# Performance work log

Measured on AMD Instinct MI355X. Metric: run time of the kernel, lower is better.

## Reference

```python
import jax, jax.numpy as jnp
import numpy as np

BS, L, DIM, H, POS = 2, 2048, 1024, 16, 16
DH = DIM // H
SCALE = float(np.round(np.sqrt(DH), 2))  # torch code: np.round(np.sqrt(d_head), 2)


def setup_inputs() -> dict:
    key = jax.random.key(0)
    ks = jax.random.split(key, 12)
    init = lambda k, shape: (jax.random.normal(k, shape, dtype=jnp.float32) * 0.02)
    inp = {
        "q": jax.random.normal(ks[0], (BS, L, DIM + POS), dtype=jnp.float32),
        "k": jax.random.normal(ks[1], (BS, L, DIM + POS), dtype=jnp.float32),
        "v": jax.random.normal(ks[2], (BS, L, DIM + POS), dtype=jnp.float32),
        "Wq": init(ks[3], (DIM, DIM)), "bq": jnp.zeros((DIM,), jnp.float32),
        "Wk": init(ks[4], (DIM, DIM)), "bk": jnp.zeros((DIM,), jnp.float32),
        "Wv": init(ks[5], (DIM, DIM)), "bv": jnp.zeros((DIM,), jnp.float32),
        "Wo": init(ks[6], (DIM, DIM)), "bo": jnp.zeros((DIM,), jnp.float32),
        # causal mask: positions with mask==1 are filled with -1e9 (strict upper triangle)
        "attn_mask": jnp.triu(jnp.ones((L, L), jnp.int32), k=1),
        "pos_token_dim": POS,
    }
    return inp


def reference(q, k, v, Wq, bq, Wk, bk, Wv, bv, Wo, bo, attn_mask, pos_token_dim):
    # pos-token suffix: stripped from q/k/v; encoding taken from k's suffix
    encoding = k[..., -pos_token_dim:]                      # [bs, L, pos]
    q = q[..., :-pos_token_dim]
    k = k[..., :-pos_token_dim]
    v = v[..., :-pos_token_dim]
    bs, Ln, dim = q.shape
    h, dh = H, DH

    # QKV projections (torch Linear: x @ W.T + b), split into heads -> [bs, h, L, dh]
    queries = (q @ Wq.T + bq).reshape(bs, Ln, h, dh).transpose(0, 2, 1, 3)
    keys    = (k @ Wk.T + bk).reshape(bs, Ln, h, dh).transpose(0, 2, 1, 3)
    values  = (v @ Wv.T + bv).reshape(bs, Ln, h, dh).transpose(0, 2, 1, 3)

    # full L x L score matrix (faithful to original naive attention)
    scores = jnp.einsum("bhld,bhmd->bhlm", queries, keys) / SCALE
    scores = jnp.where(attn_mask[None, None, :, :] == 1, jnp.float32(-1e9), scores)
    factors = jax.nn.softmax(scores, axis=-1)               # [bs, h, L, L]

    context = jnp.einsum("bhlm,bhmd->bhld", factors, values)
    context = context.transpose(0, 2, 1, 3).reshape(bs, Ln, dim)
    context = context @ Wo.T + bo                           # [bs, L, dim]

    # pos-token passthrough: attend encoding with same factors, mean over heads
    context_encoding = jnp.einsum("bhlm,bmp->bhlp", factors, encoding).mean(axis=1)
    return jnp.concatenate([context, context_encoding], axis=-1)  # [bs, L, dim+pos]
```

## Files before the change

### kernel.cpp

```cpp
#include <hip/hip_runtime.h>
#include <hip/hip_bf16.h>

#define BS   2
#define LEN  2048
#define DIM  1024
#define NH   16
#define DHD  64
#define POSD 16
#define DHE  80
#define NTOK 4096
#define INW  1040

typedef __attribute__((ext_vector_type(8))) short bf16x8;
typedef __attribute__((ext_vector_type(4))) float f32x4;

__device__ __forceinline__ short f2bf(float f) {
    union { float f; unsigned u; } v; v.f = f;
    unsigned r = v.u + 0x7fffu + ((v.u >> 16) & 1u);
    return (short)(r >> 16);
}
__device__ __forceinline__ float bf2f(short s) {
    union { unsigned u; float f; } v; v.u = ((unsigned)(unsigned short)s) << 16;
    return v.f;
}
__device__ __forceinline__ unsigned packbf(float a, float b) {
    union { float f; unsigned u; } x, y; x.f = a; y.f = b;
    return ((x.u + 0x8000u) >> 16) | ((y.u + 0x8000u) & 0xFFFF0000u);
}
__device__ __forceinline__ f32x4 mfma16(bf16x8 a, bf16x8 b, f32x4 c) {
    return __builtin_amdgcn_mfma_f32_16x16x32_bf16(a, b, c, 0, 0, 0);
}
__device__ __forceinline__ void gld16(const short* g, short* l) {
    __builtin_amdgcn_global_load_lds(
        (const __attribute__((address_space(1))) unsigned int*)g,
        (__attribute__((address_space(3))) unsigned int*)l,
        16, 0, 0);
}

__global__ __launch_bounds__(256) void prep_kernel(
    const float* __restrict__ qin, const float* __restrict__ kin, const float* __restrict__ vin,
    const float* __restrict__ Wq, const float* __restrict__ Wk,
    const float* __restrict__ Wv, const float* __restrict__ Wo,
    short* __restrict__ X16, short* __restrict__ W16, short* __restrict__ Vt)
{
    const int NA = 3 * NTOK * DIM / 4;
    const int NW = 4 * DIM * DIM / 4;
    int idx = blockIdx.x * 256 + threadIdx.x;
    if (idx < NA) {
        int per = NTOK * DIM / 4;
        int mi = idx / per, r = idx % per;
        int tok = r >> 8, c4 = r & 255;
        const float* src = (mi == 0 ? qin : (mi == 1 ? kin : vin));
        float4 v = *(const float4*)(src + (size_t)tok * INW + c4 * 4);
        short4 o;
        o.x = f2bf(v.x); o.y = f2bf(v.y); o.z = f2bf(v.z); o.w = f2bf(v.w);
        *(short4*)(X16 + (size_t)mi * NTOK * DIM + (size_t)tok * DIM + c4 * 4) = o;
        return;
    }
    idx -= NA;
    if (idx < NW) {
        int wi = idx >> 18, r = idx & 262143;
        const float* w = (wi == 0 ? Wq : (wi == 1 ? Wk : (wi == 2 ? Wv : Wo)));
        float4 v = *(const float4*)(w + (size_t)r * 4);
        short4 o;
        o.x = f2bf(v.x); o.y = f2bf(v.y); o.z = f2bf(v.z); o.w = f2bf(v.w);
        *(short4*)(W16 + (size_t)wi * DIM * DIM + (size_t)r * 4) = o;
        return;
    }
    idx -= NW;
    if (idx < BS * NH * POSD * (LEN / 8)) {
        int l8 = idx & 255;
        int p  = (idx >> 8) & 15;
        int h  = (idx >> 12) & 15;
        int b  = (idx >> 16);
        int l0 = l8 * 8;
        bf16x8 o;
        for (int i = 0; i < 8; i++)
            o[i] = f2bf(kin[(size_t)(b * LEN + l0 + i) * INW + DIM + p]);
        *(bf16x8*)(Vt + ((size_t)(b * NH + h) * DHE + DHD + p) * LEN + l0) = o;
    }
}

__global__ __launch_bounds__(256) void qkv_gemm(
    const short* __restrict__ X16, const short* __restrict__ W16,
    const float* __restrict__ bq, const float* __restrict__ bk, const float* __restrict__ bv,
    short* __restrict__ Qb, short* __restrict__ Kb, short* __restrict__ Vt)
{
    __shared__ __align__(16) short smem[24576];

    int sw = (blockIdx.x & 7) * 96 + (blockIdx.x >> 3);
    int nt = sw % 24, mt = sw / 24;
    int mat = nt >> 3, ntl = nt & 7;
    const short* A = X16 + (size_t)mat * NTOK * DIM;
    const short* W = W16 + (size_t)mat * DIM * DIM;

    int t = threadIdx.x;
    int w = t >> 6, lane = t & 63, g = lane >> 4, c = lane & 15;
    int wr = w >> 1, wc = w & 1;

    f32x4 acc[4][4];
    #pragma unroll
    for (int i = 0; i < 4; i++)
        #pragma unroll
        for (int j = 0; j < 4; j++)
            acc[i][j] = (f32x4){0.f, 0.f, 0.f, 0.f};

    int row0 = t >> 2, blk0 = t & 3;
    const short* aSrc0 = A + (size_t)(mt * 128 + row0) * DIM + blk0 * 8;
    const short* aSrc1 = aSrc0 + (size_t)64 * DIM;
    const short* bSrc0 = W + (size_t)(ntl * 128 + row0) * DIM + blk0 * 8;
    const short* bSrc1 = bSrc0 + (size_t)64 * DIM;

    short* bufC  = smem;
    short* bufN  = smem + 8192;
    short* bufNN = smem + 16384;

    {
        short* ab = bufC + w * 512;
        gld16(aSrc0, ab);
        gld16(aSrc1, ab + 2048);
        gld16(bSrc0, ab + 4096);
        gld16(bSrc1, ab + 6144);
        ab = bufN + w * 512;
        gld16(aSrc0 + 32, ab);
        gld16(aSrc1 + 32, ab + 2048);
        gld16(bSrc0 + 32, ab + 4096);
        gld16(bSrc1 + 32, ab + 6144);
    }

    for (int k = 0; k < 32; k++) {
        if (k < 30) {
            int k0 = (k + 2) * 32;
            short* ab = bufNN + w * 512;
            gld16(aSrc0 + k0, ab);
            gld16(aSrc1 + k0, ab + 2048);
            gld16(bSrc0 + k0, ab + 4096);
            gld16(bSrc1 + k0, ab + 6144);
            asm volatile("s_waitcnt vmcnt(8)" ::: "memory");
        } else if (k == 30) {
            asm volatile("s_waitcnt vmcnt(4)" ::: "memory");
        } else {
            asm volatile("s_waitcnt vmcnt(0)" ::: "memory");
        }
        __builtin_amdgcn_s_barrier();
        asm volatile("" ::: "memory");

        const short* Asb = bufC;
        const short* Bsb = bufC + 4096;
        bf16x8 af[4], bfr[4];
        #pragma unroll
        for (int fm = 0; fm < 4; fm++)
            af[fm] = *(const bf16x8*)(Asb + (wr * 64 + fm * 16 + c) * 32 + g * 8);
        #pragma unroll
        for (int fn = 0; fn < 4; fn++)
            bfr[fn] = *(const bf16x8*)(Bsb + (wc * 64 + fn * 16 + c) * 32 + g * 8);
        __builtin_amdgcn_s_setprio(1);
        #pragma unroll
        for (int fm = 0; fm < 4; fm++)
            #pragma unroll
            for (int fn = 0; fn < 4; fn++)
                acc[fm][fn] = mfma16(af[fm], bfr[fn], acc[fm][fn]);
        __builtin_amdgcn_s_setprio(0);

        asm volatile("s_waitcnt lgkmcnt(0)" ::: "memory");
        __builtin_amdgcn_s_barrier();
        asm volatile("" ::: "memory");

        short* tmp = bufC; bufC = bufN; bufN = bufNN; bufNN = tmp;
    }

    const float* bias = (mat == 0 ? bq : (mat == 1 ? bk : bv));
    if (mat == 2) {
        __syncthreads();
        #pragma unroll
        for (int fn = 0; fn < 4; fn++) {
            int nl = wc * 64 + fn * 16 + c;
            float bval = bias[ntl * 128 + nl];
            #pragma unroll
            for (int fm = 0; fm < 4; fm++) {
                int m0 = wr * 64 + fm * 16 + g * 4;
                short4 pk;
                pk.x = f2bf(acc[fm][fn][0] + bval);
                pk.y = f2bf(acc[fm][fn][1] + bval);
                pk.z = f2bf(acc[fm][fn][2] + bval);
                pk.w = f2bf(acc[fm][fn][3] + bval);
                *(short4*)(smem + nl * 136 + m0) = pk;
            }
        }
        __syncthreads();
        int b_ = (mt * 128) >> 11;
        int l0 = (mt * 128) & 2047;
        #pragma unroll
        for (int rep = 0; rep < 8; rep++) {
            int idx = rep * 256 + t;
            int row = idx >> 4, ch = idx & 15;
            bf16x8 v = *(const bf16x8*)(smem + row * 136 + ch * 8);
            int ng = ntl * 128 + row, h = ng >> 6, dh = ng & 63;
            *(bf16x8*)(Vt + ((size_t)(b_ * NH + h) * DHE + dh) * LEN + l0 + ch * 8) = v;
        }
    } else {
        float qs = (mat == 0) ? 0.18033688011112042f : 1.0f;
        short* dst = (mat == 0) ? Qb : Kb;
        #pragma unroll
        for (int fn = 0; fn < 4; fn++) {
            int n = ntl * 128 + wc * 64 + fn * 16 + c;
            float bval = bias[n];
            int h = n >> 6, dh = n & 63;
            #pragma unroll
            for (int fm = 0; fm < 4; fm++) {
                int mbase = mt * 128 + wr * 64 + fm * 16 + g * 4;
                #pragma unroll
                for (int i = 0; i < 4; i++) {
                    int m = mbase + i;
                    int b_ = m >> 11, l = m & 2047;
                    dst[((size_t)(b_ * NH + h) * LEN + l) * DHD + dh] =
                        f2bf((acc[fm][fn][i] + bval) * qs);
                }
            }
        }
    }
}

__global__ __launch_bounds__(256) void attn_kernel(
    const short* __restrict__ Qb, const short* __restrict__ Kb,
    const short* __restrict__ Vt, short* __restrict__ Ctx)
{
    __shared__ __align__(16) short Ks[64 * 64];
    __shared__ __align__(16) short Vs[DHE * 64];
    __shared__ __align__(16) short Ps[4][16 * 64];

    int bid = blockIdx.x;
    int u = bid >> 5, bh = bid & 31;
    int qt = (u < 16) ? (2 * u) : (63 - 2 * u);
    int b = bh >> 4, h = bh & 15;
    int q0 = qt * 64;
    int t = threadIdx.x, w = t >> 6, lane = t & 63, g = lane >> 4, c = lane & 15;
    const size_t bhQ = (size_t)(b * NH + h) * LEN;
    const size_t bhV = (size_t)(b * NH + h) * DHE;

    bf16x8 qa0, qa1;
    {
        const short* qp = Qb + (bhQ + q0 + w * 16 + c) * DHD;
        qa0 = *(const bf16x8*)(qp + g * 8);
        qa1 = *(const bf16x8*)(qp + 32 + g * 8);
    }

    int rK = t >> 3, blkS = t & 7;
    int swzS = (blkS ^ (rK & 7)) * 8;
    short* kDst0 = Ks + rK * 64 + swzS;
    short* kDst1 = Ks + (rK + 32) * 64 + swzS;
    short* vDst0 = Vs + rK * 64 + swzS;
    short* vDst1 = Vs + (rK + 32) * 64 + swzS;
    short* vDst2 = Vs + (rK + 64) * 64 + swzS;
    const short* kS0 = Kb + (bhQ + rK) * DHD + blkS * 8;
    const short* kS1 = Kb + (bhQ + rK + 32) * DHD + blkS * 8;
    const short* vS0 = Vt + (bhV + rK) * LEN + blkS * 8;
    const short* vS1 = Vt + (bhV + rK + 32) * LEN + blkS * 8;
    const short* vS2 = Vt + (bhV + rK + 64) * LEN + blkS * 8;
    bool v2on = (t < 128);

    {
        bf16x8 a0 = *(const bf16x8*)kS0;
        bf16x8 a1 = *(const bf16x8*)kS1;
        bf16x8 x0 = *(const bf16x8*)vS0;
        bf16x8 x1 = *(const bf16x8*)vS1;
        bf16x8 x2;
        if (v2on) x2 = *(const bf16x8*)vS2;
        *(bf16x8*)kDst0 = a0;
        *(bf16x8*)kDst1 = a1;
        *(bf16x8*)vDst0 = x0;
        *(bf16x8*)vDst1 = x1;
        if (v2on) *(bf16x8*)vDst2 = x2;
    }
    __syncthreads();

    float mrun = -1e30f, lrun = 0.f;
    f32x4 o[5];
    #pragma unroll
    for (int i = 0; i < 5; i++) o[i] = (f32x4){0.f, 0.f, 0.f, 0.f};

    for (int tt = 0; tt <= qt; tt++) {
        bf16x8 kr0, kr1, vr0, vr1, vr2;
        bool pref = (tt < qt);
        if (pref) {
            int kvn = (tt + 1) * 64;
            kr0 = *(const bf16x8*)(kS0 + (size_t)kvn * DHD);
            kr1 = *(const bf16x8*)(kS1 + (size_t)kvn * DHD);
            vr0 = *(const bf16x8*)(vS0 + kvn);
            vr1 = *(const bf16x8*)(vS1 + kvn);
            if (v2on) vr2 = *(const bf16x8*)(vS2 + kvn);
        }

        f32x4 st[4];
        __builtin_amdgcn_s_setprio(1);
        #pragma unroll
        for (int fn = 0; fn < 4; fn++) {
            int row = fn * 16 + c, sw2 = row & 7;
            bf16x8 ka = *(const bf16x8*)(Ks + row * 64 + ((g ^ sw2) * 8));
            bf16x8 kb2 = *(const bf16x8*)(Ks + row * 64 + (((4 + g) ^ sw2) * 8));
            f32x4 z = (f32x4){0.f, 0.f, 0.f, 0.f};
            z = mfma16(ka, qa0, z);
            z = mfma16(kb2, qa1, z);
            st[fn] = z;
        }
        __builtin_amdgcn_s_setprio(0);

        if (tt == qt) {
            #pragma unroll
            for (int fn = 0; fn < 4; fn++)
                #pragma unroll
                for (int i = 0; i < 4; i++)
                    if (fn * 16 + g * 4 + i > w * 16 + c) st[fn][i] = -1e9f;
        }

        float mx = st[0][0];
        #pragma unroll
        for (int fn = 0; fn < 4; fn++)
            #pragma unroll
            for (int i = 0; i < 4; i++)
                mx = fmaxf(mx, st[fn][i]);
        mx = fmaxf(mx, __shfl_xor(mx, 16));
        mx = fmaxf(mx, __shfl_xor(mx, 32));
        float mnew = fmaxf(mrun, mx);
        float scl = __builtin_amdgcn_exp2f(mrun - mnew);
        mrun = mnew;
        float ps = 0.f;
        #pragma unroll
        for (int fn = 0; fn < 4; fn++)
            #pragma unroll
            for (int i = 0; i < 4; i++) {
                float p = __builtin_amdgcn_exp2f(st[fn][i] - mnew);
                st[fn][i] = p;
                ps += p;
            }
        ps += __shfl_xor(ps, 16);
        ps += __shfl_xor(ps, 32);
        lrun = lrun * scl + ps;

        short* pw = Ps[w];
        #pragma unroll
        for (int fn = 0; fn < 4; fn++) {
            uint2 pu;
            pu.x = packbf(st[fn][0], st[fn][1]);
            pu.y = packbf(st[fn][2], st[fn][3]);
            *(uint2*)(pw + c * 64 + ((((fn << 1) | (g >> 1)) ^ (c & 7)) << 3) + ((g & 1) << 2)) = pu;
        }
        bf16x8 pa0 = *(const bf16x8*)(pw + c * 64 + ((g ^ (c & 7)) * 8));
        bf16x8 pa1 = *(const bf16x8*)(pw + c * 64 + (((4 + g) ^ (c & 7)) * 8));

        float s0 = __shfl(scl, g * 4 + 0);
        float s1 = __shfl(scl, g * 4 + 1);
        float s2 = __shfl(scl, g * 4 + 2);
        float s3 = __shfl(scl, g * 4 + 3);
        #pragma unroll
        for (int fd = 0; fd < 5; fd++) {
            o[fd][0] *= s0; o[fd][1] *= s1; o[fd][2] *= s2; o[fd][3] *= s3;
        }

        __builtin_amdgcn_s_setprio(1);
        #pragma unroll
        for (int fd = 0; fd < 5; fd++) {
            int d = fd * 16 + c, sw2 = d & 7;
            bf16x8 vb0 = *(const bf16x8*)(Vs + d * 64 + ((g ^ sw2) * 8));
            bf16x8 vb1 = *(const bf16x8*)(Vs + d * 64 + (((4 + g) ^ sw2) * 8));
            o[fd] = mfma16(pa0, vb0, o[fd]);
            o[fd] = mfma16(pa1, vb1, o[fd]);
        }
        __builtin_amdgcn_s_setprio(0);

        __syncthreads();
        if (pref) {
            *(bf16x8*)kDst0 = kr0;
            *(bf16x8*)kDst1 = kr1;
            *(bf16x8*)vDst0 = vr0;
            *(bf16x8*)vDst1 = vr1;
            if (v2on) *(bf16x8*)vDst2 = vr2;
        }
        __syncthreads();
    }

    float l0 = __shfl(lrun, g * 4 + 0);
    float l1 = __shfl(lrun, g * 4 + 1);
    float l2 = __shfl(lrun, g * 4 + 2);
    float l3 = __shfl(lrun, g * 4 + 3);
    float inv[4] = {1.f / l0, 1.f / l1, 1.f / l2, 1.f / l3};
    #pragma unroll
    for (int i = 0; i < 4; i++) {
        int q = q0 + w * 16 + g * 4 + i;
        size_t base = (bhQ + q) * DHE;
        #pragma unroll
        for (int fd = 0; fd < 5; fd++)
            Ctx[base + fd * 16 + c] = f2bf(o[fd][i] * inv[i]);
    }
}

__global__ __launch_bounds__(256) void out_gemm(
    const short* __restrict__ Ctx, const short* __restrict__ Wo16,
    const float* __restrict__ bo, float* __restrict__ out)
{
    __shared__ __align__(16) short smem[24576];

    int sw = (blockIdx.x & 7) * 32 + (blockIdx.x >> 3);
    int nt = sw & 7, mt = sw >> 3;
    int t = threadIdx.x;
    int w = t >> 6, lane = t & 63, g = lane >> 4, c = lane & 15;
    int wr = w >> 1, wc = w & 1;

    f32x4 acc[4][4];
    #pragma unroll
    for (int i = 0; i < 4; i++)
        #pragma unroll
        for (int j = 0; j < 4; j++)
            acc[i][j] = (f32x4){0.f, 0.f, 0.f, 0.f};

    int row0 = t >> 2, blk0 = t & 3;
    int tokS = mt * 128 + row0;
    int bS = tokS >> 11, lS = tokS & 2047;
    const short* aBase = Ctx + ((size_t)(bS * NH) * LEN + lS) * DHE + blk0 * 8;
    const short* aBase1 = Ctx + ((size_t)(((tokS + 64) >> 11) * NH) * LEN + ((tokS + 64) & 2047)) * DHE + blk0 * 8;
    const short* bSrc0 = Wo16 + (size_t)(nt * 128 + row0) * DIM + blk0 * 8;
    const short* bSrc1 = bSrc0 + (size_t)64 * DIM;

    short* bufC  = smem;
    short* bufN  = smem + 8192;
    short* bufNN = smem + 16384;

    {
        short* ab = bufC + w * 512;
        gld16(aBase, ab);
        gld16(aBase1, ab + 2048);
        gld16(bSrc0, ab + 4096);
        gld16(bSrc1, ab + 6144);
        ab = bufN + w * 512;
        gld16(aBase + 32, ab);
        gld16(aBase1 + 32, ab + 2048);
        gld16(bSrc0 + 32, ab + 4096);
        gld16(bSrc1 + 32, ab + 6144);
    }

    for (int k = 0; k < 32; k++) {
        if (k < 30) {
            int k0 = (k + 2) * 32;
            size_t aoff = (size_t)(k0 >> 6) * LEN * DHE + (k0 & 63);
            short* ab = bufNN + w * 512;
            gld16(aBase + aoff, ab);
            gld16(aBase1 + aoff, ab + 2048);
            gld16(bSrc0 + k0, ab + 4096);
            gld16(bSrc1 + k0, ab + 6144);
            asm volatile("s_waitcnt vmcnt(8)" ::: "memory");
        } else if (k == 30) {
            asm volatile("s_waitcnt vmcnt(4)" ::: "memory");
        } else {
            asm volatile("s_waitcnt vmcnt(0)" ::: "memory");
        }
        __builtin_amdgcn_s_barrier();
        asm volatile("" ::: "memory");

        const short* Asb = bufC;
        const short* Bsb = bufC + 4096;
        bf16x8 af[4], bfr[4];
        #pragma unroll
        for (int fm = 0; fm < 4; fm++)
            af[fm] = *(const bf16x8*)(Asb + (wr * 64 + fm * 16 + c) * 32 + g * 8);
        #pragma unroll
        for (int fn = 0; fn < 4; fn++)
            bfr[fn] = *(const bf16x8*)(Bsb + (wc * 64 + fn * 16 + c) * 32 + g * 8);
        __builtin_amdgcn_s_setprio(1);
        #pragma unroll
        for (int fm = 0; fm < 4; fm++)
            #pragma unroll
            for (int fn = 0; fn < 4; fn++)
                acc[fm][fn] = mfma16(af[fm], bfr[fn], acc[fm][fn]);
        __builtin_amdgcn_s_setprio(0);

        asm volatile("s_waitcnt lgkmcnt(0)" ::: "memory");
        __builtin_amdgcn_s_barrier();
        asm volatile("" ::: "memory");

        short* tmp = bufC; bufC = bufN; bufN = bufNN; bufNN = tmp;
    }

    #pragma unroll
    for (int fn = 0; fn < 4; fn++) {
        int n = nt * 128 + wc * 64 + fn * 16 + c;
        float bval = bo[n];
        #pragma unroll
        for (int fm = 0; fm < 4; fm++) {
            int mbase = mt * 128 + wr * 64 + fm * 16 + g * 4;
            #pragma unroll
            for (int i = 0; i < 4; i++)
                out[(size_t)(mbase + i) * INW + n] = acc[fm][fn][i] + bval;
        }
    }
}

__global__ __launch_bounds__(256) void encmean_kernel(
    const short* __restrict__ Ctx, float* __restrict__ out)
{
    int idx = blockIdx.x * 256 + threadIdx.x;
    int tok = idx >> 4, p = idx & 15;
    int b = tok >> 11, l = tok & 2047;
    float s = 0.f;
    #pragma unroll
    for (int h = 0; h < NH; h++)
        s += bf2f(Ctx[((size_t)(b * NH + h) * LEN + l) * DHE + DHD + p]);
    out[(size_t)tok * INW + DIM + p] = s * (1.0f / NH);
}

extern "C" void kernel_launch(void* const* d_in, const int* in_sizes, int n_in,
                              void* d_out, int out_size, void* d_ws, size_t ws_size,
                              hipStream_t stream)
{
    const float* qin = (const float*)d_in[0];
    const float* kin = (const float*)d_in[1];
    const float* vin = (const float*)d_in[2];
    const float* Wq  = (const float*)d_in[3];
    const float* bq  = (const float*)d_in[4];
    const float* Wk  = (const float*)d_in[5];
    const float* bk  = (const float*)d_in[6];
    const float* Wv  = (const float*)d_in[7];
    const float* bv  = (const float*)d_in[8];
    const float* Wo  = (const float*)d_in[9];
    const float* bo  = (const float*)d_in[10];
    float* out = (float*)d_out;

    short* X16 = (short*)d_ws;
    short* W16 = X16 + (size_t)3 * NTOK * DIM;
    short* Qb  = W16 + (size_t)4 * DIM * DIM;
    short* Kb  = Qb  + (size_t)NTOK * DIM;
    short* Vt  = Kb  + (size_t)NTOK * DIM;
    short* Ctx = Vt  + (size_t)BS * NH * DHE * LEN;

    prep_kernel<<<16896, 256, 0, stream>>>(qin, kin, vin, Wq, Wk, Wv, Wo, X16, W16, Vt);
    qkv_gemm<<<768, 256, 0, stream>>>(X16, W16, bq, bk, bv, Qb, Kb, Vt);
    attn_kernel<<<1024, 256, 0, stream>>>(Qb, Kb, Vt, Ctx);
    out_gemm<<<256, 256, 0, stream>>>(Ctx, W16 + (size_t)3 * DIM * DIM, bo, out);
    encmean_kernel<<<256, 256, 0, stream>>>(Ctx, out);
}
```

Measured before the change: 132.6 us.

## Restructure attention so each wave owns 32 query rows and reads K/V from global

Attention is reorganised so each wave works independently on 32 query rows, two 16-row sub-tiles, of its own (batch, head). The wave loads K and V fragments straight from global memory into registers and prefetches the next tile itself, so the shared-memory K/V staging and both block-wide barriers per iteration are gone. The grid is halved and launch bounds now ask for two blocks per CU. Waves in a block now serve different heads and query tiles, so K/V data is no longer shared through LDS and global/L2 traffic per FLOP rises; register pressure also grows with the doubled accumulators and the register-held K/V.

Result: slower. 183.9 us (+38.7%).

```diff
diff --git a/kernel.cpp b/kernel.cpp
--- a/kernel.cpp
+++ b/kernel.cpp
@@ -221,176 +221,182 @@
     }
 }
 
-__global__ __launch_bounds__(256) void attn_kernel(
+__global__ __launch_bounds__(256, 2) void attn_kernel(
     const short* __restrict__ Qb, const short* __restrict__ Kb,
     const short* __restrict__ Vt, short* __restrict__ Ctx)
 {
-    __shared__ __align__(16) short Ks[64 * 64];
-    __shared__ __align__(16) short Vs[DHE * 64];
-    __shared__ __align__(16) short Ps[4][16 * 64];
+    __shared__ __align__(16) short Ps[4][2048];
 
     int bid = blockIdx.x;
-    int u = bid >> 5, bh = bid & 31;
-    int qt = (u < 16) ? (2 * u) : (63 - 2 * u);
+    int p = 31 - (bid >> 4);
+    int bhp = bid & 15;
+    int t = threadIdx.x, w = t >> 6, lane = t & 63, g = lane >> 4, c = lane & 15;
+    int bh = bhp + ((w & 1) << 4);
+    int W = 2 * p + (w >> 1);
     int b = bh >> 4, h = bh & 15;
-    int q0 = qt * 64;
-    int t = threadIdx.x, w = t >> 6, lane = t & 63, g = lane >> 4, c = lane & 15;
+    int wq0 = W * 32;
+    int T = p + 1;
     const size_t bhQ = (size_t)(b * NH + h) * LEN;
     const size_t bhV = (size_t)(b * NH + h) * DHE;
-
-    bf16x8 qa0, qa1;
-    {
-        const short* qp = Qb + (bhQ + q0 + w * 16 + c) * DHD;
-        qa0 = *(const bf16x8*)(qp + g * 8);
-        qa1 = *(const bf16x8*)(qp + 32 + g * 8);
-    }
-
-    int rK = t >> 3, blkS = t & 7;
-    int swzS = (blkS ^ (rK & 7)) * 8;
-    short* kDst0 = Ks + rK * 64 + swzS;
-    short* kDst1 = Ks + (rK + 32) * 64 + swzS;
-    short* vDst0 = Vs + rK * 64 + swzS;
-    short* vDst1 = Vs + (rK + 32) * 64 + swzS;
-    short* vDst2 = Vs + (rK + 64) * 64 + swzS;
-    const short* kS0 = Kb + (bhQ + rK) * DHD + blkS * 8;
-    const short* kS1 = Kb + (bhQ + rK + 32) * DHD + blkS * 8;
-    const short* vS0 = Vt + (bhV + rK) * LEN + blkS * 8;
-    const short* vS1 = Vt + (bhV + rK + 32) * LEN + blkS * 8;
-    const short* vS2 = Vt + (bhV + rK + 64) * LEN + blkS * 8;
-    bool v2on = (t < 128);
-
-    {
-        bf16x8 a0 = *(const bf16x8*)kS0;
-        bf16x8 a1 = *(const bf16x8*)kS1;
-        bf16x8 x0 = *(const bf16x8*)vS0;
-        bf16x8 x1 = *(const bf16x8*)vS1;
-        bf16x8 x2;
-        if (v2on) x2 = *(const bf16x8*)vS2;
-        *(bf16x8*)kDst0 = a0;
-        *(bf16x8*)kDst1 = a1;
-        *(bf16x8*)vDst0 = x0;
-        *(bf16x8*)vDst1 = x1;
-        if (v2on) *(bf16x8*)vDst2 = x2;
-    }
-    __syncthreads();
-
-    float mrun = -1e30f, lrun = 0.f;
-    f32x4 o[5];
-    #pragma unroll
-    for (int i = 0; i < 5; i++) o[i] = (f32x4){0.f, 0.f, 0.f, 0.f};
-
-    for (int tt = 0; tt <= qt; tt++) {
-        bf16x8 kr0, kr1, vr0, vr1, vr2;
-        bool pref = (tt < qt);
-        if (pref) {
+    short* pw = Ps[w];
+
+    bf16x8 qa[2][2];
+    #pragma unroll
+    for (int h2 = 0; h2 < 2; h2++)
+        #pragma unroll
+        for (int ks = 0; ks < 2; ks++)
+            qa[h2][ks] = *(const bf16x8*)(Qb + (bhQ + wq0 + h2 * 16 + c) * DHD + ks * 32 + g * 8);
+
+    const short* kB = Kb + (bhQ + c) * DHD + g * 8;
+    const short* vB = Vt + (bhV + c) * LEN + g * 8;
+
+    bf16x8 ka[4][2], vb[5][2];
+    #pragma unroll
+    for (int fn = 0; fn < 4; fn++)
+        #pragma unroll
+        for (int ks = 0; ks < 2; ks++)
+            ka[fn][ks] = *(const bf16x8*)(kB + (size_t)(fn * 16) * DHD + ks * 32);
+    #pragma unroll
+    for (int fd = 0; fd < 5; fd++)
+        #pragma unroll
+        for (int ks = 0; ks < 2; ks++)
+            vb[fd][ks] = *(const bf16x8*)(vB + (size_t)(fd * 16) * LEN + ks * 32);
+
+    float mrun[2] = {-1e30f, -1e30f}, lrun[2] = {0.f, 0.f};
+    f32x4 o[2][5];
+    #pragma unroll
+    for (int h2 = 0; h2 < 2; h2++)
+        #pragma unroll
+        for (int fd = 0; fd < 5; fd++)
+            o[h2][fd] = (f32x4){0.f, 0.f, 0.f, 0.f};
+
+    for (int tt = 0; tt < T; tt++) {
+        f32x4 st[2][4];
+        __builtin_amdgcn_s_setprio(1);
+        #pragma unroll
+        for (int h2 = 0; h2 < 2; h2++)
+            #pragma unroll
+            for (int fn = 0; fn < 4; fn++) {
+                f32x4 z = (f32x4){0.f, 0.f, 0.f, 0.f};
+                z = mfma16(ka[fn][0], qa[h2][0], z);
+                z = mfma16(ka[fn][1], qa[h2][1], z);
+                st[h2][fn] = z;
+            }
+        __builtin_amdgcn_s_setprio(0);
+
+        if (tt + 1 < T) {
             int kvn = (tt + 1) * 64;
-            kr0 = *(const bf16x8*)(kS0 + (size_t)kvn * DHD);
-            kr1 = *(const bf16x8*)(kS1 + (size_t)kvn * DHD);
-            vr0 = *(const bf16x8*)(vS0 + kvn);
-            vr1 = *(const bf16x8*)(vS1 + kvn);
-            if (v2on) vr2 = *(const bf16x8*)(vS2 + kvn);
-        }
-
-        f32x4 st[4];
-        __builtin_amdgcn_s_setprio(1);
-        #pragma unroll
-        for (int fn = 0; fn < 4; fn++) {
-            int row = fn * 16 + c, sw2 = row & 7;
-            bf16x8 ka = *(const bf16x8*)(Ks + row * 64 + ((g ^ sw2) * 8));
-            bf16x8 kb2 = *(const bf16x8*)(Ks + row * 64 + (((4 + g) ^ sw2) * 8));
-            f32x4 z = (f32x4){0.f, 0.f, 0.f, 0.f};
-            z = mfma16(ka, qa0, z);
-            z = mfma16(kb2, qa1, z);
-            st[fn] = z;
-        }
-        __builtin_amdgcn_s_setprio(0);
-
-        if (tt == qt) {
+            #pragma unroll
+            for (int fn = 0; fn < 4; fn++)
+                #pragma unroll
+                for (int ks = 0; ks < 2; ks++)
+                    ka[fn][ks] = *(const bf16x8*)(kB + (size_t)(kvn + fn * 16) * DHD + ks * 32);
+        }
+
+        if (tt == T - 1) {
+            #pragma unroll
+            for (int h2 = 0; h2 < 2; h2++)
+                #pragma unroll
+                for (int fn = 0; fn < 4; fn++)
+                    #pragma unroll
+                    for (int i = 0; i < 4; i++)
+                        if (tt * 64 + fn * 16 + g * 4 + i > wq0 + h2 * 16 + c)
+                            st[h2][fn][i] = -1e30f;
+        }
+
+        float scl[2];
+        #pragma unroll
+        for (int h2 = 0; h2 < 2; h2++) {
+            float mx = st[h2][0][0];
             #pragma unroll
             for (int fn = 0; fn < 4; fn++)
                 #pragma unroll
                 for (int i = 0; i < 4; i++)
-                    if (fn * 16 + g * 4 + i > w * 16 + c) st[fn][i] = -1e9f;
-        }
-
-        float mx = st[0][0];
-        #pragma unroll
-        for (int fn = 0; fn < 4; fn++)
-            #pragma unroll
-            for (int i = 0; i < 4; i++)
-                mx = fmaxf(mx, st[fn][i]);
-        mx = fmaxf(mx, __shfl_xor(mx, 16));
-        mx = fmaxf(mx, __shfl_xor(mx, 32));
-        float mnew = fmaxf(mrun, mx);
-        float scl = __builtin_amdgcn_exp2f(mrun - mnew);
-        mrun = mnew;
-        float ps = 0.f;
-        #pragma unroll
-        for (int fn = 0; fn < 4; fn++)
-            #pragma unroll
-            for (int i = 0; i < 4; i++) {
-                float p = __builtin_amdgcn_exp2f(st[fn][i] - mnew);
-                st[fn][i] = p;
-                ps += p;
+                    mx = fmaxf(mx, st[h2][fn][i]);
+            mx = fmaxf(mx, __shfl_xor(mx, 16));
+            mx = fmaxf(mx, __shfl_xor(mx, 32));
+            float mnew = fmaxf(mrun[h2], mx);
+            scl[h2] = __builtin_amdgcn_exp2f(mrun[h2] - mnew);
+            mrun[h2] = mnew;
+            float ps = 0.f;
+            #pragma unroll
+            for (int fn = 0; fn < 4; fn++)
+                #pragma unroll
+                for (int i = 0; i < 4; i++) {
+                    float pe = __builtin_amdgcn_exp2f(st[h2][fn][i] - mnew);
+                    st[h2][fn][i] = pe;
+                    ps += pe;
+                }
+            ps += __shfl_xor(ps, 16);
+            ps += __shfl_xor(ps, 32);
+            lrun[h2] = lrun[h2] * scl[h2] + ps;
+        }
+
+        #pragma unroll
+        for (int h2 = 0; h2 < 2; h2++)
+            #pragma unroll
+            for (int fn = 0; fn < 4; fn++) {
+                uint2 pu;
+                pu.x = packbf(st[h2][fn][0], st[h2][fn][1]);
+                pu.y = packbf(st[h2][fn][2], st[h2][fn][3]);
+                *(uint2*)(pw + (h2 * 16 + c) * 64 +
+                          ((((fn << 1) | (g >> 1)) ^ (c & 7)) << 3) + ((g & 1) << 2)) = pu;
             }
-        ps += __shfl_xor(ps, 16);
-        ps += __shfl_xor(ps, 32);
-        lrun = lrun * scl + ps;
-
-        short* pw = Ps[w];
-        #pragma unroll
-        for (int fn = 0; fn < 4; fn++) {
-            uint2 pu;
-            pu.x = packbf(st[fn][0], st[fn][1]);
-            pu.y = packbf(st[fn][2], st[fn][3]);
-            *(uint2*)(pw + c * 64 + ((((fn << 1) | (g >> 1)) ^ (c & 7)) << 3) + ((g & 1) << 2)) = pu;
-        }
-        bf16x8 pa0 = *(const bf16x8*)(pw + c * 64 + ((g ^ (c & 7)) * 8));
-        bf16x8 pa1 = *(const bf16x8*)(pw + c * 64 + (((4 + g) ^ (c & 7)) * 8));
-
-        float s0 = __shfl(scl, g * 4 + 0);
-        float s1 = __shfl(scl, g * 4 + 1);
-        float s2 = __shfl(scl, g * 4 + 2);
-        float s3 = __shfl(scl, g * 4 + 3);
-        #pragma unroll
-        for (int fd = 0; fd < 5; fd++) {
-            o[fd][0] *= s0; o[fd][1] *= s1; o[fd][2] *= s2; o[fd][3] *= s3;
+        bf16x8 pa[2][2];
+        #pragma unroll
+        for (int h2 = 0; h2 < 2; h2++) {
+            pa[h2][0] = *(const bf16x8*)(pw + (h2 * 16 + c) * 64 + ((g ^ (c & 7)) * 8));
+            pa[h2][1] = *(const bf16x8*)(pw + (h2 * 16 + c) * 64 + (((4 + g) ^ (c & 7)) * 8));
+        }
+
+        #pragma unroll
+        for (int h2 = 0; h2 < 2; h2++) {
+            float s0 = __shfl(scl[h2], g * 4 + 0);
+            float s1 = __shfl(scl[h2], g * 4 + 1);
+            float s2 = __shfl(scl[h2], g * 4 + 2);
+            float s3 = __shfl(scl[h2], g * 4 + 3);
+            #pragma unroll
+            for (int fd = 0; fd < 5; fd++) {
+                o[h2][fd][0] *= s0; o[h2][fd][1] *= s1;
+                o[h2][fd][2] *= s2; o[h2][fd][3] *= s3;
+            }
         }
 
         __builtin_amdgcn_s_setprio(1);
         #pragma unroll
-        for (int fd = 0; fd < 5; fd++) {
-            int d = fd * 16 + c, sw2 = d & 7;
-            bf16x8 vb0 = *(const bf16x8*)(Vs + d * 64 + ((g ^ sw2) * 8));
-            bf16x8 vb1 = *(const bf16x8*)(Vs + d * 64 + (((4 + g) ^ sw2) * 8));
-            o[fd] = mfma16(pa0, vb0, o[fd]);
-            o[fd] = mfma16(pa1, vb1, o[fd]);
-        }
+        for (int h2 = 0; h2 < 2; h2++)
+            #pragma unroll
+            for (int fd = 0; fd < 5; fd++) {
+                o[h2][fd] = mfma16(pa[h2][0], vb[fd][0], o[h2][fd]);
+                o[h2][fd] = mfma16(pa[h2][1], vb[fd][1], o[h2][fd]);
+            }
         __builtin_amdgcn_s_setprio(0);
 
-        __syncthreads();
-        if (pref) {
-            *(bf16x8*)kDst0 = kr0;
-            *(bf16x8*)kDst1 = kr1;
-            *(bf16x8*)vDst0 = vr0;
-            *(bf16x8*)vDst1 = vr1;
-            if (v2on) *(bf16x8*)vDst2 = vr2;
-        }
-        __syncthreads();
-    }
-
-    float l0 = __shfl(lrun, g * 4 + 0);
-    float l1 = __shfl(lrun, g * 4 + 1);
-    float l2 = __shfl(lrun, g * 4 + 2);
-    float l3 = __shfl(lrun, g * 4 + 3);
-    float inv[4] = {1.f / l0, 1.f / l1, 1.f / l2, 1.f / l3};
-    #pragma unroll
-    for (int i = 0; i < 4; i++) {
-        int q = q0 + w * 16 + g * 4 + i;
-        size_t base = (bhQ + q) * DHE;
-        #pragma unroll
-        for (int fd = 0; fd < 5; fd++)
-            Ctx[base + fd * 16 + c] = f2bf(o[fd][i] * inv[i]);
+        if (tt + 1 < T) {
+            int kvn = (tt + 1) * 64;
+            #pragma unroll
+            for (int fd = 0; fd < 5; fd++)
+                #pragma unroll
+                for (int ks = 0; ks < 2; ks++)
+                    vb[fd][ks] = *(const bf16x8*)(vB + (size_t)(fd * 16) * LEN + kvn + ks * 32);
+        }
+    }
+
+    #pragma unroll
+    for (int h2 = 0; h2 < 2; h2++) {
+        float l0 = __shfl(lrun[h2], g * 4 + 0);
+        float l1 = __shfl(lrun[h2], g * 4 + 1);
+        float l2 = __shfl(lrun[h2], g * 4 + 2);
+        float l3 = __shfl(lrun[h2], g * 4 + 3);
+        float inv[4] = {1.f / l0, 1.f / l1, 1.f / l2, 1.f / l3};
+        #pragma unroll
+        for (int i = 0; i < 4; i++) {
+            int q = wq0 + h2 * 16 + g * 4 + i;
+            size_t base = (bhQ + q) * DHE;
+            #pragma unroll
+            for (int fd = 0; fd < 5; fd++)
+                Ctx[base + fd * 16 + c] = f2bf(o[h2][fd][i] * inv[i]);
+        }
     }
 }
 
@@ -533,7 +539,7 @@
 
     prep_kernel<<<16896, 256, 0, stream>>>(qin, kin, vin, Wq, Wk, Wv, Wo, X16, W16, Vt);
     qkv_gemm<<<768, 256, 0, stream>>>(X16, W16, bq, bk, bv, Qb, Kb, Vt);
-    attn_kernel<<<1024, 256, 0, stream>>>(Qb, Kb, Vt, Ctx);
+    attn_kernel<<<512, 256, 0, stream>>>(Qb, Kb, Vt, Ctx);
     out_gemm<<<256, 256, 0, stream>>>(Ctx, W16 + (size_t)3 * DIM * DIM, bo, out);
     encmean_kernel<<<256, 256, 0, stream>>>(Ctx, out);
 }
```

## Rework attention onto 32x32 MFMA with register-resident P and lazy rescaling

Applied to the files above, without the earlier changes.

The attention kernel moves from 16x16x32 to 32x32x16 bf16 MFMA. Each block now has two waves, and each wave owns 32 query rows. The probability tile is repacked across lanes with cross-half shuffles instead of a round trip through LDS, and the online-softmax rescale of the accumulators is skipped unless the running max grows by more than 8. Query tiles are scheduled longest-first to shrink the tail, which in exchange brings fewer threads per block, higher register pressure and wasted MFMA work on padded V rows.

Result: slower. 182.1 us (+37.4%).

```diff
diff --git a/kernel.cpp b/kernel.cpp
--- a/kernel.cpp
+++ b/kernel.cpp
@@ -13,6 +13,8 @@
 
 typedef __attribute__((ext_vector_type(8))) short bf16x8;
 typedef __attribute__((ext_vector_type(4))) float f32x4;
+typedef __attribute__((ext_vector_type(16))) float f32x16;
+typedef __attribute__((ext_vector_type(4))) unsigned uint32x4;
 
 __device__ __forceinline__ short f2bf(float f) {
     union { float f; unsigned u; } v; v.f = f;
@@ -29,6 +31,9 @@
 }
 __device__ __forceinline__ f32x4 mfma16(bf16x8 a, bf16x8 b, f32x4 c) {
     return __builtin_amdgcn_mfma_f32_16x16x32_bf16(a, b, c, 0, 0, 0);
+}
+__device__ __forceinline__ f32x16 mfma32(bf16x8 a, bf16x8 b, f32x16 c) {
+    return __builtin_amdgcn_mfma_f32_32x32x16_bf16(a, b, c, 0, 0, 0);
 }
 __device__ __forceinline__ void gld16(const short* g, short* l) {
     __builtin_amdgcn_global_load_lds(
@@ -221,176 +226,211 @@
     }
 }
 
-__global__ __launch_bounds__(256) void attn_kernel(
+__global__ __launch_bounds__(128) void attn_kernel(
     const short* __restrict__ Qb, const short* __restrict__ Kb,
     const short* __restrict__ Vt, short* __restrict__ Ctx)
 {
     __shared__ __align__(16) short Ks[64 * 64];
-    __shared__ __align__(16) short Vs[DHE * 64];
-    __shared__ __align__(16) short Ps[4][16 * 64];
+    __shared__ __align__(16) short Vs[96 * 64];
 
     int bid = blockIdx.x;
     int u = bid >> 5, bh = bid & 31;
-    int qt = (u < 16) ? (2 * u) : (63 - 2 * u);
+    int qt = (u < 16) ? (31 - 2 * u) : (2 * u - 32);
     int b = bh >> 4, h = bh & 15;
     int q0 = qt * 64;
-    int t = threadIdx.x, w = t >> 6, lane = t & 63, g = lane >> 4, c = lane & 15;
+    int t = threadIdx.x, w = t >> 6, l = t & 63;
+    int q32 = l & 31, half = l >> 5;
+    int wq0 = q0 + w * 32;
+    int T = qt + 1;
     const size_t bhQ = (size_t)(b * NH + h) * LEN;
     const size_t bhV = (size_t)(b * NH + h) * DHE;
 
-    bf16x8 qa0, qa1;
+    bf16x8 qf[4];
+    #pragma unroll
+    for (int dks = 0; dks < 4; dks++)
+        qf[dks] = *(const bf16x8*)(Qb + (bhQ + wq0 + q32) * DHD + dks * 16 + half * 8);
+
+    int sr = t >> 3, sb = t & 7;
+    int ssw = (sb ^ (sr & 7)) * 8;
+    const short* kS0 = Kb + (bhQ + sr) * DHD + sb * 8;
+    const short* kS1 = kS0 + (size_t)16 * DHD;
+    const short* kS2 = kS0 + (size_t)32 * DHD;
+    const short* kS3 = kS0 + (size_t)48 * DHD;
+    short* kD0 = Ks + sr * 64 + ssw;
+    short* kD1 = kD0 + 16 * 64;
+    short* kD2 = kD0 + 32 * 64;
+    short* kD3 = kD0 + 48 * 64;
+    const short* vS0 = Vt + (bhV + sr) * LEN + sb * 8;
+    const short* vS1 = vS0 + (size_t)16 * LEN;
+    const short* vS2 = vS0 + (size_t)32 * LEN;
+    const short* vS3 = vS0 + (size_t)48 * LEN;
+    const short* vS4 = vS0 + (size_t)64 * LEN;
+    short* vD0 = Vs + sr * 64 + ssw;
+    short* vD1 = vD0 + 16 * 64;
+    short* vD2 = vD0 + 32 * 64;
+    short* vD3 = vD0 + 48 * 64;
+    short* vD4 = vD0 + 64 * 64;
+
     {
-        const short* qp = Qb + (bhQ + q0 + w * 16 + c) * DHD;
-        qa0 = *(const bf16x8*)(qp + g * 8);
-        qa1 = *(const bf16x8*)(qp + 32 + g * 8);
-    }
-
-    int rK = t >> 3, blkS = t & 7;
-    int swzS = (blkS ^ (rK & 7)) * 8;
-    short* kDst0 = Ks + rK * 64 + swzS;
-    short* kDst1 = Ks + (rK + 32) * 64 + swzS;
-    short* vDst0 = Vs + rK * 64 + swzS;
-    short* vDst1 = Vs + (rK + 32) * 64 + swzS;
-    short* vDst2 = Vs + (rK + 64) * 64 + swzS;
-    const short* kS0 = Kb + (bhQ + rK) * DHD + blkS * 8;
-    const short* kS1 = Kb + (bhQ + rK + 32) * DHD + blkS * 8;
-    const short* vS0 = Vt + (bhV + rK) * LEN + blkS * 8;
-    const short* vS1 = Vt + (bhV + rK + 32) * LEN + blkS * 8;
-    const short* vS2 = Vt + (bhV + rK + 64) * LEN + blkS * 8;
-    bool v2on = (t < 128);
-
-    {
-        bf16x8 a0 = *(const bf16x8*)kS0;
-        bf16x8 a1 = *(const bf16x8*)kS1;
-        bf16x8 x0 = *(const bf16x8*)vS0;
-        bf16x8 x1 = *(const bf16x8*)vS1;
-        bf16x8 x2;
-        if (v2on) x2 = *(const bf16x8*)vS2;
-        *(bf16x8*)kDst0 = a0;
-        *(bf16x8*)kDst1 = a1;
-        *(bf16x8*)vDst0 = x0;
-        *(bf16x8*)vDst1 = x1;
-        if (v2on) *(bf16x8*)vDst2 = x2;
+        bf16x8 a0 = *(const bf16x8*)kS0, a1 = *(const bf16x8*)kS1;
+        bf16x8 a2 = *(const bf16x8*)kS2, a3 = *(const bf16x8*)kS3;
+        bf16x8 x0 = *(const bf16x8*)vS0, x1 = *(const bf16x8*)vS1;
+        bf16x8 x2 = *(const bf16x8*)vS2, x3 = *(const bf16x8*)vS3;
+        bf16x8 x4 = *(const bf16x8*)vS4;
+        *(bf16x8*)kD0 = a0; *(bf16x8*)kD1 = a1;
+        *(bf16x8*)kD2 = a2; *(bf16x8*)kD3 = a3;
+        *(bf16x8*)vD0 = x0; *(bf16x8*)vD1 = x1;
+        *(bf16x8*)vD2 = x2; *(bf16x8*)vD3 = x3;
+        *(bf16x8*)vD4 = x4;
     }
     __syncthreads();
 
     float mrun = -1e30f, lrun = 0.f;
-    f32x4 o[5];
-    #pragma unroll
-    for (int i = 0; i < 5; i++) o[i] = (f32x4){0.f, 0.f, 0.f, 0.f};
-
-    for (int tt = 0; tt <= qt; tt++) {
-        bf16x8 kr0, kr1, vr0, vr1, vr2;
-        bool pref = (tt < qt);
+    f32x16 o0, o1, o2;
+    #pragma unroll
+    for (int r = 0; r < 16; r++) { o0[r] = 0.f; o1[r] = 0.f; o2[r] = 0.f; }
+
+    int swq = (q32 & 7);
+
+    for (int tt = 0; tt < T; tt++) {
+        int kv0 = tt * 64;
+        bf16x8 kr0, kr1, kr2, kr3, vr0, vr1, vr2, vr3, vr4;
+        bool pref = (tt + 1 < T);
         if (pref) {
-            int kvn = (tt + 1) * 64;
-            kr0 = *(const bf16x8*)(kS0 + (size_t)kvn * DHD);
-            kr1 = *(const bf16x8*)(kS1 + (size_t)kvn * DHD);
-            vr0 = *(const bf16x8*)(vS0 + kvn);
-            vr1 = *(const bf16x8*)(vS1 + kvn);
-            if (v2on) vr2 = *(const bf16x8*)(vS2 + kvn);
-        }
-
-        f32x4 st[4];
+            size_t ko = (size_t)(kv0 + 64) * DHD;
+            int vo = kv0 + 64;
+            kr0 = *(const bf16x8*)(kS0 + ko); kr1 = *(const bf16x8*)(kS1 + ko);
+            kr2 = *(const bf16x8*)(kS2 + ko); kr3 = *(const bf16x8*)(kS3 + ko);
+            vr0 = *(const bf16x8*)(vS0 + vo); vr1 = *(const bf16x8*)(vS1 + vo);
+            vr2 = *(const bf16x8*)(vS2 + vo); vr3 = *(const bf16x8*)(vS3 + vo);
+            vr4 = *(const bf16x8*)(vS4 + vo);
+        }
+
+        f32x16 s0, s1;
+        #pragma unroll
+        for (int r = 0; r < 16; r++) { s0[r] = 0.f; s1[r] = 0.f; }
         __builtin_amdgcn_s_setprio(1);
         #pragma unroll
-        for (int fn = 0; fn < 4; fn++) {
-            int row = fn * 16 + c, sw2 = row & 7;
-            bf16x8 ka = *(const bf16x8*)(Ks + row * 64 + ((g ^ sw2) * 8));
-            bf16x8 kb2 = *(const bf16x8*)(Ks + row * 64 + (((4 + g) ^ sw2) * 8));
-            f32x4 z = (f32x4){0.f, 0.f, 0.f, 0.f};
-            z = mfma16(ka, qa0, z);
-            z = mfma16(kb2, qa1, z);
-            st[fn] = z;
+        for (int dks = 0; dks < 4; dks++) {
+            int ch = dks * 2 + half;
+            bf16x8 ka0 = *(const bf16x8*)(Ks + q32 * 64 + ((ch ^ swq) * 8));
+            bf16x8 ka1 = *(const bf16x8*)(Ks + (32 + q32) * 64 + ((ch ^ swq) * 8));
+            s0 = mfma32(ka0, qf[dks], s0);
+            s1 = mfma32(ka1, qf[dks], s1);
         }
         __builtin_amdgcn_s_setprio(0);
 
-        if (tt == qt) {
-            #pragma unroll
-            for (int fn = 0; fn < 4; fn++)
-                #pragma unroll
-                for (int i = 0; i < 4; i++)
-                    if (fn * 16 + g * 4 + i > w * 16 + c) st[fn][i] = -1e9f;
-        }
-
-        float mx = st[0][0];
-        #pragma unroll
-        for (int fn = 0; fn < 4; fn++)
-            #pragma unroll
-            for (int i = 0; i < 4; i++)
-                mx = fmaxf(mx, st[fn][i]);
-        mx = fmaxf(mx, __shfl_xor(mx, 16));
+        if (kv0 + 63 > wq0) {
+            int qg = wq0 + q32;
+            #pragma unroll
+            for (int r = 0; r < 16; r++) {
+                int kvl = (r & 3) + 8 * (r >> 2) + 4 * half;
+                if (kv0 + kvl > qg) s0[r] = -1e30f;
+                if (kv0 + 32 + kvl > qg) s1[r] = -1e30f;
+            }
+        }
+
+        float mx = s0[0];
+        #pragma unroll
+        for (int r = 0; r < 16; r++) { mx = fmaxf(mx, s0[r]); mx = fmaxf(mx, s1[r]); }
         mx = fmaxf(mx, __shfl_xor(mx, 32));
-        float mnew = fmaxf(mrun, mx);
-        float scl = __builtin_amdgcn_exp2f(mrun - mnew);
-        mrun = mnew;
+
         float ps = 0.f;
-        #pragma unroll
-        for (int fn = 0; fn < 4; fn++)
-            #pragma unroll
-            for (int i = 0; i < 4; i++) {
-                float p = __builtin_amdgcn_exp2f(st[fn][i] - mnew);
-                st[fn][i] = p;
-                ps += p;
+        if (__all(mx <= mrun + 8.f)) {
+            #pragma unroll
+            for (int r = 0; r < 16; r++) {
+                float a = __builtin_amdgcn_exp2f(s0[r] - mrun);
+                float c = __builtin_amdgcn_exp2f(s1[r] - mrun);
+                s0[r] = a; s1[r] = c; ps += a + c;
             }
-        ps += __shfl_xor(ps, 16);
+        } else {
+            float mnew = fmaxf(mrun, mx);
+            float scl = __builtin_amdgcn_exp2f(mrun - mnew);
+            mrun = mnew;
+            #pragma unroll
+            for (int r = 0; r < 16; r++) {
+                float a = __builtin_amdgcn_exp2f(s0[r] - mnew);
+                float c = __builtin_amdgcn_exp2f(s1[r] - mnew);
+                s0[r] = a; s1[r] = c; ps += a + c;
+            }
+            lrun *= scl;
+            #pragma unroll
+            for (int r = 0; r < 16; r++) {
+                float sc = __shfl(scl, (r & 3) + 8 * (r >> 2) + 4 * half);
+                o0[r] *= sc; o1[r] *= sc; o2[r] *= sc;
+            }
+        }
         ps += __shfl_xor(ps, 32);
-        lrun = lrun * scl + ps;
-
-        short* pw = Ps[w];
-        #pragma unroll
-        for (int fn = 0; fn < 4; fn++) {
-            uint2 pu;
-            pu.x = packbf(st[fn][0], st[fn][1]);
-            pu.y = packbf(st[fn][2], st[fn][3]);
-            *(uint2*)(pw + c * 64 + ((((fn << 1) | (g >> 1)) ^ (c & 7)) << 3) + ((g & 1) << 2)) = pu;
-        }
-        bf16x8 pa0 = *(const bf16x8*)(pw + c * 64 + ((g ^ (c & 7)) * 8));
-        bf16x8 pa1 = *(const bf16x8*)(pw + c * 64 + (((4 + g) ^ (c & 7)) * 8));
-
-        float s0 = __shfl(scl, g * 4 + 0);
-        float s1 = __shfl(scl, g * 4 + 1);
-        float s2 = __shfl(scl, g * 4 + 2);
-        float s3 = __shfl(scl, g * 4 + 3);
-        #pragma unroll
-        for (int fd = 0; fd < 5; fd++) {
-            o[fd][0] *= s0; o[fd][1] *= s1; o[fd][2] *= s2; o[fd][3] *= s3;
+        lrun += ps;
+
+        unsigned tA0 = packbf(s0[0], s0[1]),  tA1 = packbf(s0[2], s0[3]);
+        unsigned tA2 = packbf(s0[4], s0[5]),  tA3 = packbf(s0[6], s0[7]);
+        unsigned tA4 = packbf(s0[8], s0[9]),  tA5 = packbf(s0[10], s0[11]);
+        unsigned tA6 = packbf(s0[12], s0[13]), tA7 = packbf(s0[14], s0[15]);
+        unsigned tB0 = packbf(s1[0], s1[1]),  tB1 = packbf(s1[2], s1[3]);
+        unsigned tB2 = packbf(s1[4], s1[5]),  tB3 = packbf(s1[6], s1[7]);
+        unsigned tB4 = packbf(s1[8], s1[9]),  tB5 = packbf(s1[10], s1[11]);
+        unsigned tB6 = packbf(s1[12], s1[13]), tB7 = packbf(s1[14], s1[15]);
+
+        bf16x8 pa0, pa1, pa2, pa3;
+        {
+            unsigned xA0 = __shfl_xor((int)tA0, 32), xA1 = __shfl_xor((int)tA1, 32);
+            unsigned xA2 = __shfl_xor((int)tA2, 32), xA3 = __shfl_xor((int)tA3, 32);
+            unsigned xA4 = __shfl_xor((int)tA4, 32), xA5 = __shfl_xor((int)tA5, 32);
+            unsigned xA6 = __shfl_xor((int)tA6, 32), xA7 = __shfl_xor((int)tA7, 32);
+            uint32x4 P;
+            P.x = half ? xA2 : tA0; P.y = half ? xA3 : tA1;
+            P.z = half ? tA2 : xA0; P.w = half ? tA3 : xA1;
+            pa0 = *(bf16x8*)&P;
+            P.x = half ? xA6 : tA4; P.y = half ? xA7 : tA5;
+            P.z = half ? tA6 : xA4; P.w = half ? tA7 : xA5;
+            pa1 = *(bf16x8*)&P;
+            unsigned xB0 = __shfl_xor((int)tB0, 32), xB1 = __shfl_xor((int)tB1, 32);
+            unsigned xB2 = __shfl_xor((int)tB2, 32), xB3 = __shfl_xor((int)tB3, 32);
+            unsigned xB4 = __shfl_xor((int)tB4, 32), xB5 = __shfl_xor((int)tB5, 32);
+            unsigned xB6 = __shfl_xor((int)tB6, 32), xB7 = __shfl_xor((int)tB7, 32);
+            P.x = half ? xB2 : tB0; P.y = half ? xB3 : tB1;
+            P.z = half ? tB2 : xB0; P.w = half ? tB3 : xB1;
+            pa2 = *(bf16x8*)&P;
+            P.x = half ? xB6 : tB4; P.y = half ? xB7 : tB5;
+            P.z = half ? tB6 : xB4; P.w = half ? tB7 : xB5;
+            pa3 = *(bf16x8*)&P;
         }
 
         __builtin_amdgcn_s_setprio(1);
         #pragma unroll
-        for (int fd = 0; fd < 5; fd++) {
-            int d = fd * 16 + c, sw2 = d & 7;
-            bf16x8 vb0 = *(const bf16x8*)(Vs + d * 64 + ((g ^ sw2) * 8));
-            bf16x8 vb1 = *(const bf16x8*)(Vs + d * 64 + (((4 + g) ^ sw2) * 8));
-            o[fd] = mfma16(pa0, vb0, o[fd]);
-            o[fd] = mfma16(pa1, vb1, o[fd]);
+        for (int ks = 0; ks < 4; ks++) {
+            bf16x8 pk = (ks == 0) ? pa0 : (ks == 1) ? pa1 : (ks == 2) ? pa2 : pa3;
+            int ch = ks * 2 + half;
+            bf16x8 v0 = *(const bf16x8*)(Vs + q32 * 64 + ((ch ^ swq) * 8));
+            bf16x8 v1 = *(const bf16x8*)(Vs + (32 + q32) * 64 + ((ch ^ swq) * 8));
+            bf16x8 v2 = *(const bf16x8*)(Vs + (64 + q32) * 64 + ((ch ^ swq) * 8));
+            o0 = mfma32(pk, v0, o0);
+            o1 = mfma32(pk, v1, o1);
+            o2 = mfma32(pk, v2, o2);
         }
         __builtin_amdgcn_s_setprio(0);
 
         __syncthreads();
         if (pref) {
-            *(bf16x8*)kDst0 = kr0;
-            *(bf16x8*)kDst1 = kr1;
-            *(bf16x8*)vDst0 = vr0;
-            *(bf16x8*)vDst1 = vr1;
-            if (v2on) *(bf16x8*)vDst2 = vr2;
+            *(bf16x8*)kD0 = kr0; *(bf16x8*)kD1 = kr1;
+            *(bf16x8*)kD2 = kr2; *(bf16x8*)kD3 = kr3;
+            *(bf16x8*)vD0 = vr0; *(bf16x8*)vD1 = vr1;
+            *(bf16x8*)vD2 = vr2; *(bf16x8*)vD3 = vr3;
+            *(bf16x8*)vD4 = vr4;
         }
         __syncthreads();
     }
 
-    float l0 = __shfl(lrun, g * 4 + 0);
-    float l1 = __shfl(lrun, g * 4 + 1);
-    float l2 = __shfl(lrun, g * 4 + 2);
-    float l3 = __shfl(lrun, g * 4 + 3);
-    float inv[4] = {1.f / l0, 1.f / l1, 1.f / l2, 1.f / l3};
-    #pragma unroll
-    for (int i = 0; i < 4; i++) {
-        int q = q0 + w * 16 + g * 4 + i;
-        size_t base = (bhQ + q) * DHE;
-        #pragma unroll
-        for (int fd = 0; fd < 5; fd++)
-            Ctx[base + fd * 16 + c] = f2bf(o[fd][i] * inv[i]);
+    float inv = 1.f / lrun;
+    #pragma unroll
+    for (int r = 0; r < 16; r++) {
+        int qloc = (r & 3) + 8 * (r >> 2) + 4 * half;
+        float iv = __shfl(inv, qloc);
+        size_t base = (bhQ + wq0 + qloc) * DHE;
+        Ctx[base + q32]      = f2bf(o0[r] * iv);
+        Ctx[base + 32 + q32] = f2bf(o1[r] * iv);
+        if (q32 < 16) Ctx[base + 64 + q32] = f2bf(o2[r] * iv);
     }
 }
 
@@ -533,7 +573,7 @@
 
     prep_kernel<<<16896, 256, 0, stream>>>(qin, kin, vin, Wq, Wk, Wv, Wo, X16, W16, Vt);
     qkv_gemm<<<768, 256, 0, stream>>>(X16, W16, bq, bk, bv, Qb, Kb, Vt);
-    attn_kernel<<<1024, 256, 0, stream>>>(Qb, Kb, Vt, Ctx);
+    attn_kernel<<<1024, 128, 0, stream>>>(Qb, Kb, Vt, Ctx);
     out_gemm<<<256, 256, 0, stream>>>(Ctx, W16 + (size_t)3 * DIM * DIM, bo, out);
     encmean_kernel<<<256, 256, 0, stream>>>(Ctx, out);
 }
```
